# Optimization experiments

Hardware: AMD Instinct MI355X
Metric: run time of the kernel (lower is better)

Reference implementation:

```python
import jax, jax.numpy as jnp
import numpy as np

EPS = 1e-12      # F.normalize eps
BN_EPS = 1e-5    # BatchNorm1d eps


def _l2norm(x):
    # x: (B, E, S); normalize over channel dim E (torch F.normalize default dim=1)
    n = jnp.sqrt(jnp.sum(x * x, axis=1, keepdims=True))
    return x / jnp.maximum(n, EPS)


def _conv1x1(w, b, x):
    # 1x1 Conv1d: w (O, E), b (O,), x (B, S, E) -> (B, O, S)
    return jnp.einsum('oe,bse->bos', w, x) + b[None, :, None]


def _batchnorm(x, g, b):
    # train-mode BatchNorm1d on (B, F): biased batch stats over dim 0
    m = jnp.mean(x, axis=0)
    v = jnp.var(x, axis=0)
    return (x - m) * jax.lax.rsqrt(v + BN_EPS) * g + b


def _pairwise(X, Y, wx, bx, wy, by, g, be, mxw, mxb, myw, myb):
    # X: (B, Sx, e), Y: (B, Sy, e)
    Xn = _l2norm(_conv1x1(wx, bx, X))           # (B, E, Sx)
    Yn = _l2norm(_conv1x1(wy, by, Y))           # (B, E, Sy)
    S = jnp.einsum('bex,bey->bxy', Xn, Yn)       # (B, Sx, Sy)
    B, Sx, Sy = S.shape
    S = _batchnorm(S.reshape(B, Sx * Sy), g, be).reshape(B, Sx, Sy)
    potX = jnp.einsum('y,bxy->bx', mxw, S) + mxb  # margin_X: Conv1d(Sy,1,1)
    potY = jnp.einsum('x,bxy->by', myw, S) + myb  # margin_Y: Conv1d(Sx,1,1)
    return potX, potY


def _pairwise_self(X, wx, bx, wy, by, g, be, mxw, mxb):
    # Pairwise with Y=None: embed_X and embed_Y both applied to X; only X_poten returned
    Xn = _l2norm(_conv1x1(wx, bx, X))
    Yn = _l2norm(_conv1x1(wy, by, X))
    S = jnp.einsum('bex,bey->bxy', Xn, Yn)
    B, Sx, Sy = S.shape
    S = _batchnorm(S.reshape(B, Sx * Sy), g, be).reshape(B, Sx, Sy)
    return jnp.einsum('y,bxy->bx', mxw, S) + mxb


def _unary(X, w1, b1, w2, b2):
    # Unary: conv1d e->e, relu, (dropout=identity in eval), conv1d e->1
    h = jax.nn.relu(_conv1x1(w1, b1, X))         # (B, E, S)
    return jnp.einsum('e,bes->bs', w2, h) + b2


def _forward(utils, un_w1, un_b1, un_w2, un_b2,
             sp_wx, sp_bx, sp_wy, sp_by, sp_g, sp_b, sp_mxw, sp_mxb,
             pw_wx, pw_bx, pw_wy, pw_by, pw_g, pw_b, pw_mxw, pw_mxb, pw_myw, pw_myb,
             red_w):
    # utils: (3, B, S, e)
    unp = jax.vmap(_unary)(utils, un_w1, un_b1, un_w2, un_b2)                    # (3, B, S)
    sfp = jax.vmap(_pairwise_self)(utils, sp_wx, sp_bx, sp_wy, sp_by,
                                   sp_g, sp_b, sp_mxw, sp_mxb)                   # (3, B, S)
    # pairwise pairs in combinations order: (0,1), (0,2), (1,2)
    idx_i = jnp.array([0, 0, 1])
    idx_j = jnp.array([1, 2, 2])
    pX, pY = jax.vmap(_pairwise)(utils[idx_i], utils[idx_j],
                                 pw_wx, pw_bx, pw_wy, pw_by, pw_g, pw_b,
                                 pw_mxw, pw_mxb, pw_myw, pw_myb)                 # (3, B, S) each
    pots = [
        [unp[0], sfp[0], pX[0], pX[1]],   # util 0: ij of (0,1), ij of (0,2)
        [unp[1], sfp[1], pY[0], pX[2]],   # util 1: ji of (0,1), ij of (1,2)
        [unp[2], sfp[2], pY[1], pY[2]],   # util 2: ji of (0,2), ji of (1,2)
    ]
    outs = []
    for i in range(3):
        P = jnp.stack(pots[i], axis=1)                 # (B, 4, S)
        red = jnp.einsum('k,bks->bs', red_w[i], P)     # Conv1d(4,1,1,bias=False)
        attn = jax.nn.softmax(red, axis=1)             # softmax over spatial dim
        outs.append(jnp.einsum('bse,bs->be', utils[i], attn))  # bmm(utils^T, attn)
    return jnp.stack(outs, axis=0)                     # (3, B, e)


def setup_inputs() -> dict:
    key = jax.random.key(0)
    ks = iter(jax.random.split(key, 32))
    def rn(shape, scale=0.05):
        return jax.random.normal(next(ks), shape, dtype=jnp.float32) * scale
    e, S, B, NU, NP = 128, 1024, 32, 3, 3
    F = S * S
    return dict(
        utils=rn((NU, B, S, e), 1.0),
        un_w1=rn((NU, e, e)), un_b1=rn((NU, e)), un_w2=rn((NU, e)), un_b2=rn((NU,)),
        sp_wx=rn((NU, e, e)), sp_bx=rn((NU, e)), sp_wy=rn((NU, e, e)), sp_by=rn((NU, e)),
        sp_g=jnp.ones((NU, F), jnp.float32), sp_b=jnp.zeros((NU, F), jnp.float32),
        sp_mxw=rn((NU, S)), sp_mxb=rn((NU,)),
        pw_wx=rn((NP, e, e)), pw_bx=rn((NP, e)), pw_wy=rn((NP, e, e)), pw_by=rn((NP, e)),
        pw_g=jnp.ones((NP, F), jnp.float32), pw_b=jnp.zeros((NP, F), jnp.float32),
        pw_mxw=rn((NP, S)), pw_mxb=rn((NP,)), pw_myw=rn((NP, S)), pw_myb=rn((NP,)),
        red_w=rn((NU, 4)),
    )


def reference(utils, un_w1, un_b1, un_w2, un_b2,
              sp_wx, sp_bx, sp_wy, sp_by, sp_g, sp_b, sp_mxw, sp_mxb,
              pw_wx, pw_bx, pw_wy, pw_by, pw_g, pw_b, pw_mxw, pw_mxb, pw_myw, pw_myb,
              red_w):
    return _forward(utils, un_w1, un_b1, un_w2, un_b2,
                    sp_wx, sp_bx, sp_wy, sp_by, sp_g, sp_b, sp_mxw, sp_mxb,
                    pw_wx, pw_bx, pw_wy, pw_by, pw_g, pw_b, pw_mxw, pw_mxb, pw_myw, pw_myb,
                    red_w)
```

## Files before the change

kernel.cpp:

```cpp
#include <hip/hip_runtime.h>
#include <math.h>

constexpr int EE = 128;
constexpr int NS = 1024;
constexpr int NB = 32;
constexpr size_t BSE = (size_t)NB * NS * EE;

typedef __attribute__((ext_vector_type(4))) float f32x4;
typedef __attribute__((ext_vector_type(8))) short s16x8;
typedef __attribute__((ext_vector_type(4))) short s16x4;
typedef __attribute__((ext_vector_type(8))) __bf16 bf16v8;

__device__ __forceinline__ f32x4 mfma16(s16x8 a, s16x8 b, f32x4 c) {
  return __builtin_amdgcn_mfma_f32_16x16x32_bf16(
      __builtin_bit_cast(bf16v8, a), __builtin_bit_cast(bf16v8, b), c, 0, 0, 0);
}

__device__ __forceinline__ unsigned short f2bf(float f) {
  unsigned u = __builtin_bit_cast(unsigned, f);
  u += 0x7FFFu + ((u >> 16) & 1u);
  return (unsigned short)(u >> 16);
}
__device__ __forceinline__ float bf2f(unsigned short h) {
  unsigned u = ((unsigned)h) << 16;
  return __builtin_bit_cast(float, u);
}

__device__ __forceinline__ int swz(int b)  { return b ^ (((b >> 8) & 7) << 4); }
__device__ __forceinline__ int swz7(int b) { return b ^ (((b >> 7) & 7) << 4); }

__device__ __forceinline__ void gl_lds16(const void* gptr, void* lptr) {
  auto g = (const __attribute__((address_space(1))) unsigned int*)gptr;
  auto l = (__attribute__((address_space(3))) unsigned int*)lptr;
  __builtin_amdgcn_global_load_lds(g, l, 16, 0, 0);
}

__device__ __forceinline__ void stage32k(const char* gsrc, char* ldst, int wv, int lane) {
#pragma unroll
  for (int c = 0; c < 8; ++c) {
    int uoff = c*4096 + wv*1024;
    gl_lds16(gsrc + swz(uoff + lane*16), ldst + uoff);
  }
}

__device__ __forceinline__ void stage_half(const char* tile, char* ldst, int kh, int wv, int lane) {
#pragma unroll
  for (int c = 0; c < 4; ++c) {
    int uoff = c*4096 + wv*1024;
    int sa = swz7(uoff + lane*16);
    gl_lds16(tile + (sa >> 7)*256 + kh*128 + (sa & 127), ldst + uoff);
  }
}

constexpr size_t EMB_OFF   = 0;
constexpr size_t UNP_OFF   = EMB_OFF + 12ull * BSE * 2;
constexpr size_t SUMS_OFF  = UNP_OFF + 3ull * NB * NS * 4;
constexpr size_t SUMS2_OFF = SUMS_OFF + 6ull * NS * NS * 4;
constexpr size_t RB_OFF    = SUMS2_OFF + 6ull * NS * NS * 4;
constexpr size_t CX_OFF    = RB_OFF + 6ull * NS * NS * 2;
constexpr size_t POTX_OFF  = CX_OFF + 6ull * NS * 4;
constexpr size_t PYP_OFF   = POTX_OFF + 6ull * NB * NS * 4;
constexpr size_t CY_OFF    = PYP_OFF + 3ull * NB * 8 * NS * 4;

__global__ __launch_bounds__(256, 2) void embed_kernel(
    const float* __restrict__ utils,
    const float* __restrict__ un_w1, const float* __restrict__ un_b1,
    const float* __restrict__ un_w2, const float* __restrict__ un_b2,
    const float* __restrict__ sp_wx, const float* __restrict__ sp_bx,
    const float* __restrict__ sp_wy, const float* __restrict__ sp_by,
    const float* __restrict__ pw_wx, const float* __restrict__ pw_bx,
    const float* __restrict__ pw_wy, const float* __restrict__ pw_by,
    unsigned short* __restrict__ emb, float* __restrict__ unp)
{
  const int job = blockIdx.x >> 9;
  const int pt  = blockIdx.x & 511;
  const int u = job / 5, m = job % 5;

  const float* W; const float* bias;
  unsigned short* dst = nullptr;
  int mode;
  if (m == 0)      { W = un_w1 + u*EE*EE; bias = un_b1 + u*EE; mode = 0; }
  else if (m == 1) { W = sp_wx + u*EE*EE; bias = sp_bx + u*EE; dst = emb + (size_t)(2*u)*BSE;   mode = 1; }
  else if (m == 2) { W = sp_wy + u*EE*EE; bias = sp_by + u*EE; dst = emb + (size_t)(2*u+1)*BSE; mode = 1; }
  else {
    int q, side;
    if (u == 0)      { q = (m == 3) ? 0 : 1; side = 0; }
    else if (u == 1) { if (m == 3) { q = 0; side = 1; } else { q = 2; side = 0; } }
    else             { q = (m == 3) ? 1 : 2; side = 1; }
    W    = (side == 0 ? pw_wx : pw_wy) + q*EE*EE;
    bias = (side == 0 ? pw_bx : pw_by) + q*EE;
    dst  = emb + (size_t)(2*(3+q)+side)*BSE;
    mode = 1;
  }

  __shared__ short lA[64*128];
  __shared__ short lB[128*128];
  __shared__ float redbuf[64];

  const int t = threadIdx.x;
  {
    const char* src = (const char*)(utils + (size_t)u*BSE + (size_t)pt*64*EE);
#pragma unroll
    for (int c = 0; c < 8; ++c) {
      int off = c*4096 + t*16;
      float4 v = *(const float4*)(src + off);
      s16x4 h;
      h.x = (short)f2bf(v.x); h.y = (short)f2bf(v.y);
      h.z = (short)f2bf(v.z); h.w = (short)f2bf(v.w);
      *(s16x4*)((char*)lA + swz(off >> 1)) = h;
    }
    const char* wsrc = (const char*)W;
#pragma unroll
    for (int c = 0; c < 16; ++c) {
      int off = c*4096 + t*16;
      float4 v = *(const float4*)(wsrc + off);
      s16x4 h;
      h.x = (short)f2bf(v.x); h.y = (short)f2bf(v.y);
      h.z = (short)f2bf(v.z); h.w = (short)f2bf(v.w);
      *(s16x4*)((char*)lB + swz(off >> 1)) = h;
    }
  }
  __syncthreads();

  const int lane = t & 63, wv = t >> 6;
  const int wrE = wv & 1, wcE = wv >> 1;
  const int cL = lane & 15, r4 = (lane >> 4) * 4, k8 = (lane >> 4) * 8;

  f32x4 acc[2][4];
#pragma unroll
  for (int i = 0; i < 2; ++i)
#pragma unroll
    for (int j = 0; j < 4; ++j) acc[i][j] = f32x4{0.f, 0.f, 0.f, 0.f};

#pragma unroll
  for (int kk = 0; kk < 4; ++kk) {
    s16x8 av[2], bv[4];
#pragma unroll
    for (int i = 0; i < 2; ++i) {
      int row = wrE*32 + i*16 + cL;
      av[i] = *(const s16x8*)((const char*)lA + swz(row*256 + kk*64 + k8*2));
    }
#pragma unroll
    for (int j = 0; j < 4; ++j) {
      int row = wcE*64 + j*16 + cL;
      bv[j] = *(const s16x8*)((const char*)lB + swz(row*256 + kk*64 + k8*2));
    }
#pragma unroll
    for (int i = 0; i < 2; ++i)
#pragma unroll
      for (int j = 0; j < 4; ++j)
        acc[i][j] = mfma16(av[i], bv[j], acc[i][j]);
  }

  if (mode == 0) {
    const float* w2 = un_w2 + u*EE;
    float s[2][4];
#pragma unroll
    for (int i = 0; i < 2; ++i)
#pragma unroll
      for (int r = 0; r < 4; ++r) s[i][r] = 0.f;
#pragma unroll
    for (int i = 0; i < 2; ++i) {
#pragma unroll
      for (int j = 0; j < 4; ++j) {
        int o = wcE*64 + j*16 + cL;
        float bv2 = bias[o], w2v = w2[o];
#pragma unroll
        for (int r = 0; r < 4; ++r) {
          float v = acc[i][j][r] + bv2;
          v = v > 0.f ? v : 0.f;
          s[i][r] += v * w2v;
        }
      }
    }
#pragma unroll
    for (int msk = 1; msk < 16; msk <<= 1)
#pragma unroll
      for (int i = 0; i < 2; ++i)
#pragma unroll
        for (int r = 0; r < 4; ++r)
          s[i][r] += __shfl_xor(s[i][r], msk, 64);
    if (t < 64) redbuf[t] = 0.f;
    __syncthreads();
    if (cL == 0) {
#pragma unroll
      for (int i = 0; i < 2; ++i)
#pragma unroll
        for (int r = 0; r < 4; ++r)
          atomicAdd(&redbuf[wrE*32 + i*16 + r4 + r], s[i][r]);
    }
    __syncthreads();
    if (t < 64) unp[(size_t)u*NB*NS + (size_t)pt*64 + t] = redbuf[t] + un_b2[u];
  } else {
    float nrm[2][4];
#pragma unroll
    for (int i = 0; i < 2; ++i)
#pragma unroll
      for (int r = 0; r < 4; ++r) nrm[i][r] = 0.f;
#pragma unroll
    for (int i = 0; i < 2; ++i) {
#pragma unroll
      for (int j = 0; j < 4; ++j) {
        int o = wcE*64 + j*16 + cL;
        float bv2 = bias[o];
#pragma unroll
        for (int r = 0; r < 4; ++r) {
          acc[i][j][r] += bv2;
          nrm[i][r] += acc[i][j][r] * acc[i][j][r];
        }
      }
    }
#pragma unroll
    for (int msk = 1; msk < 16; msk <<= 1)
#pragma unroll
      for (int i = 0; i < 2; ++i)
#pragma unroll
        for (int r = 0; r < 4; ++r)
          nrm[i][r] += __shfl_xor(nrm[i][r], msk, 64);
    if (t < 64) redbuf[t] = 0.f;
    __syncthreads();
    if (cL == 0) {
#pragma unroll
      for (int i = 0; i < 2; ++i)
#pragma unroll
        for (int r = 0; r < 4; ++r)
          atomicAdd(&redbuf[wrE*32 + i*16 + r4 + r], nrm[i][r]);
    }
    __syncthreads();
#pragma unroll
    for (int i = 0; i < 2; ++i) {
#pragma unroll
      for (int r = 0; r < 4; ++r) {
        float n = redbuf[wrE*32 + i*16 + r4 + r];
        float sc = 1.f / fmaxf(sqrtf(n), 1e-12f);
        size_t pbase = ((size_t)pt*64 + wrE*32 + i*16 + r4 + r) * EE;
#pragma unroll
        for (int j = 0; j < 4; ++j) {
          int o = wcE*64 + j*16 + cL;
          dst[pbase + o] = f2bf(acc[i][j][r] * sc);
        }
      }
    }
  }
}

__global__ __launch_bounds__(256, 2) void pass1_kernel(
    const unsigned short* __restrict__ emb,
    float* __restrict__ sumS, float* __restrict__ sumS2)
{
  const int bid = blockIdx.x;
  const int p = bid >> 6, xt = (bid >> 3) & 7, yt = bid & 7;
  const char* Xe = (const char*)(emb + (size_t)(2*p)*BSE + (size_t)xt*128*EE);
  const char* Ye = (const char*)(emb + (size_t)(2*p+1)*BSE + (size_t)yt*128*EE);
  __shared__ char lds[65536];
  const int t = threadIdx.x, lane = t & 63, wv = t >> 6;
  const int wr = wv >> 1, wc = wv & 1, cL = lane & 15, r4 = (lane >> 4) * 4;
  const int q16 = (lane >> 4) * 16;

  f32x4 sS[4][4], sQ[4][4], acc[4][4];
#pragma unroll
  for (int i = 0; i < 4; ++i)
#pragma unroll
    for (int j = 0; j < 4; ++j) { sS[i][j] = f32x4{0.f,0.f,0.f,0.f}; sQ[i][j] = f32x4{0.f,0.f,0.f,0.f}; }

  stage_half(Xe, lds, 0, wv, lane);
  stage_half(Ye, lds + 16384, 0, wv, lane);
  __syncthreads();

  for (int s = 0; s < 2*NB; ++s) {
    const int cur = s & 1;
    const char* buf = lds + cur * 32768;
    if (s + 1 < 2*NB) {
      const int b1 = (s + 1) >> 1, kh1 = (s + 1) & 1;
      char* nb = lds + (cur ^ 1) * 32768;
      stage_half(Xe + (size_t)b1*NS*EE*2, nb, kh1, wv, lane);
      stage_half(Ye + (size_t)b1*NS*EE*2, nb + 16384, kh1, wv, lane);
    }
    if ((s & 1) == 0) {
#pragma unroll
      for (int i = 0; i < 4; ++i)
#pragma unroll
        for (int j = 0; j < 4; ++j) acc[i][j] = f32x4{0.f,0.f,0.f,0.f};
    }
#pragma unroll
    for (int kk2 = 0; kk2 < 2; ++kk2) {
      s16x8 av[4], bv[4];
#pragma unroll
      for (int i = 0; i < 4; ++i) {
        int row = wr*64 + i*16 + cL;
        av[i] = *(const s16x8*)(buf + swz7(row*128 + kk2*64 + q16));
      }
#pragma unroll
      for (int j = 0; j < 4; ++j) {
        int row = wc*64 + j*16 + cL;
        bv[j] = *(const s16x8*)(buf + 16384 + swz7(row*128 + kk2*64 + q16));
      }
#pragma unroll
      for (int i = 0; i < 4; ++i)
#pragma unroll
        for (int j = 0; j < 4; ++j)
          acc[i][j] = mfma16(av[i], bv[j], acc[i][j]);
    }
    if (s & 1) {
#pragma unroll
      for (int i = 0; i < 4; ++i)
#pragma unroll
        for (int j = 0; j < 4; ++j) {
          sS[i][j] += acc[i][j];
          sQ[i][j] += acc[i][j] * acc[i][j];
        }
    }
    __syncthreads();
  }
  float* oS = sumS  + (size_t)p * NS * NS;
  float* oQ = sumS2 + (size_t)p * NS * NS;
#pragma unroll
  for (int i = 0; i < 4; ++i)
#pragma unroll
    for (int j = 0; j < 4; ++j)
#pragma unroll
      for (int r = 0; r < 4; ++r) {
        int row = xt*128 + wr*64 + i*16 + r4 + r;
        int col = yt*128 + wc*64 + j*16 + cL;
        oS[(size_t)row*NS + col] = sS[i][j][r];
        oQ[(size_t)row*NS + col] = sQ[i][j][r];
      }
}

__global__ void stats_kernel(
    const float* __restrict__ sumS, const float* __restrict__ sumS2,
    const float* __restrict__ sp_g, const float* __restrict__ sp_b,
    const float* __restrict__ sp_mxw, const float* __restrict__ sp_mxb,
    const float* __restrict__ pw_g, const float* __restrict__ pw_b,
    const float* __restrict__ pw_mxw, const float* __restrict__ pw_mxb,
    unsigned short* __restrict__ Rb, float* __restrict__ cX)
{
  const int p = blockIdx.x >> 10, x = blockIdx.x & 1023, t = threadIdx.x;
  const float* g; const float* bb; const float* mxw; float mxb;
  if (p < 3) {
    g = sp_g + (size_t)p*NS*NS; bb = sp_b + (size_t)p*NS*NS;
    mxw = sp_mxw + p*NS; mxb = sp_mxb[p];
  } else {
    int q = p - 3;
    g = pw_g + (size_t)q*NS*NS; bb = pw_b + (size_t)q*NS*NS;
    mxw = pw_mxw + q*NS; mxb = pw_mxb[q];
  }
  const size_t ro = (size_t)p*NS*NS + (size_t)x*NS;
  const size_t gro = (size_t)x*NS;
  const int y = t * 4;
  float4 s4 = *(const float4*)(sumS + ro + y);
  float4 q4 = *(const float4*)(sumS2 + ro + y);
  float4 g4 = *(const float4*)(g + gro + y);
  float4 b4 = *(const float4*)(bb + gro + y);
  float4 m4 = *(const float4*)(mxw + y);
  float partial = 0.f;
  s16x4 rq;
  {
    const float inv = 1.f / 32.f;
    float sv[4] = {s4.x, s4.y, s4.z, s4.w};
    float qv[4] = {q4.x, q4.y, q4.z, q4.w};
    float gv[4] = {g4.x, g4.y, g4.z, g4.w};
    float bv[4] = {b4.x, b4.y, b4.z, b4.w};
    float mw[4] = {m4.x, m4.y, m4.z, m4.w};
#pragma unroll
    for (int c = 0; c < 4; ++c) {
      float mean = sv[c] * inv;
      float var  = qv[c] * inv - mean * mean;
      float rstd = rsqrtf(var + 1e-5f);
      unsigned short rh = f2bf(gv[c] * rstd);
      rq[c] = (short)rh;
      float Rq = bf2f(rh);
      partial += mw[c] * (bv[c] - Rq * mean);
    }
  }
  *(s16x4*)(Rb + ro + y) = rq;
  __shared__ float sred[256];
  sred[t] = partial;
  __syncthreads();
  if (t < 128) sred[t] += sred[t + 128];
  __syncthreads();
  if (t < 64) {
    float v = sred[t] + sred[t + 64];
#pragma unroll
    for (int msk = 1; msk < 64; msk <<= 1) v += __shfl_xor(v, msk, 64);
    if (t == 0) cX[p*NS + x] = v + mxb;
  }
}

__global__ __launch_bounds__(256, 4) void cy_kernel(
    const float* __restrict__ sumS, const unsigned short* __restrict__ Rb,
    const float* __restrict__ pw_b, const float* __restrict__ pw_myw,
    float* __restrict__ cY)
{
  const int q = blockIdx.x >> 4, ys = blockIdx.x & 15;
  const int p = q + 3;
  const int t = threadIdx.x, rg = t >> 6, c = t & 63;
  const int y = ys * 64 + c;
  const float* Sp = sumS + (size_t)p * NS * NS;
  const unsigned short* Rp = Rb + (size_t)p * NS * NS;
  const float* bbp = pw_b + (size_t)q * NS * NS;
  const float* myw = pw_myw + q * NS;
  const float inv = 1.f / 32.f;
  float acc = 0.f;
#pragma unroll 4
  for (int x = rg * 256; x < rg * 256 + 256; ++x) {
    float mw = myw[x];
    float mean = Sp[(size_t)x * NS + y] * inv;
    float R = bf2f(Rp[(size_t)x * NS + y]);
    float bbv = bbp[(size_t)x * NS + y];
    acc += mw * (bbv - R * mean);
  }
  __shared__ float red[256];
  red[t] = acc;
  __syncthreads();
  if (rg == 0)
    cY[(size_t)p * NS + y] = red[c] + red[64 + c] + red[128 + c] + red[192 + c];
}

__global__ __launch_bounds__(256, 2) void pass2_kernel(
    const unsigned short* __restrict__ emb, const unsigned short* __restrict__ Rb,
    const float* __restrict__ sp_mxw, const float* __restrict__ pw_mxw,
    const float* __restrict__ pw_myw,
    float* __restrict__ potX, float* __restrict__ potYpart)
{
  const int bid = blockIdx.x;
  const int p = bid >> 8, b = (bid >> 3) & 31, xt = bid & 7;
  const char* Ae = (const char*)(emb + (size_t)(2*p)*BSE + ((size_t)b*NS + (size_t)xt*128)*EE);
  const char* Be = (const char*)(emb + (size_t)(2*p+1)*BSE + (size_t)b*NS*EE);
  const unsigned short* Rp = Rb + (size_t)p*NS*NS;
  const float* mxw = (p < 3) ? (sp_mxw + p*NS) : (pw_mxw + (p-3)*NS);
  const float* myw = (p < 3) ? nullptr : (pw_myw + (p-3)*NS);
  __shared__ char lA[32768];
  __shared__ char lB[32768];
  __shared__ float pxbuf[128];
  __shared__ float pybuf[1024];
  const int t = threadIdx.x, lane = t & 63, wv = t >> 6;
  const int wr = wv >> 1, wc = wv & 1, cL = lane & 15, r4 = (lane >> 4) * 4, k8 = (lane >> 4) * 8;

  stage32k(Ae, lA, wv, lane);
  stage32k(Be, lB, wv, lane);
  if (t < 128) pxbuf[t] = 0.f;
#pragma unroll
  for (int k = 0; k < 4; ++k) pybuf[t + k*256] = 0.f;
  __syncthreads();

  float px[4][4];
#pragma unroll
  for (int i = 0; i < 4; ++i)
#pragma unroll
    for (int r = 0; r < 4; ++r) px[i][r] = 0.f;
  float mywv[4][4];
  if (myw) {
#pragma unroll
    for (int i = 0; i < 4; ++i)
#pragma unroll
      for (int r = 0; r < 4; ++r)
        mywv[i][r] = myw[xt*128 + wr*64 + i*16 + r4 + r];
  }

  for (int yt = 0; yt < 8; ++yt) {
    f32x4 acc[4][4];
#pragma unroll
    for (int i = 0; i < 4; ++i)
#pragma unroll
      for (int j = 0; j < 4; ++j) acc[i][j] = f32x4{0.f,0.f,0.f,0.f};
#pragma unroll
    for (int kk = 0; kk < 4; ++kk) {
      s16x8 av[4], bv[4];
#pragma unroll
      for (int i = 0; i < 4; ++i) {
        int row = wr*64 + i*16 + cL;
        av[i] = *(const s16x8*)(lA + swz(row*256 + kk*64 + k8*2));
      }
#pragma unroll
      for (int j = 0; j < 4; ++j) {
        int row = wc*64 + j*16 + cL;
        bv[j] = *(const s16x8*)(lB + swz(row*256 + kk*64 + k8*2));
      }
#pragma unroll
      for (int i = 0; i < 4; ++i)
#pragma unroll
        for (int j = 0; j < 4; ++j)
          acc[i][j] = mfma16(av[i], bv[j], acc[i][j]);
    }
    __syncthreads();

    float mxl[4];
#pragma unroll
    for (int j = 0; j < 4; ++j) mxl[j] = mxw[yt*128 + wc*64 + j*16 + cL];

    if (myw) {
      float py[4] = {0.f, 0.f, 0.f, 0.f};
#pragma unroll
      for (int i = 0; i < 4; ++i) {
#pragma unroll
        for (int r = 0; r < 4; ++r) {
          const unsigned short* Rr = Rp + (size_t)(xt*128 + wr*64 + i*16 + r4 + r)*NS + yt*128;
          float pxa = 0.f;
#pragma unroll
          for (int j = 0; j < 4; ++j) {
            float Rv = bf2f(Rr[wc*64 + j*16 + cL]);
            float tt = Rv * acc[i][j][r];
            pxa += mxl[j] * tt;
            py[j] += mywv[i][r] * tt;
          }
          px[i][r] += pxa;
        }
      }
#pragma unroll
      for (int j = 0; j < 4; ++j) {
        py[j] += __shfl_xor(py[j], 16, 64);
        py[j] += __shfl_xor(py[j], 32, 64);
      }
      if ((lane >> 4) == 0) {
#pragma unroll
        for (int j = 0; j < 4; ++j)
          atomicAdd(&pybuf[yt*128 + wc*64 + j*16 + cL], py[j]);
      }
    } else {
#pragma unroll
      for (int i = 0; i < 4; ++i) {
#pragma unroll
        for (int r = 0; r < 4; ++r) {
          const unsigned short* Rr = Rp + (size_t)(xt*128 + wr*64 + i*16 + r4 + r)*NS + yt*128;
          float pxa = 0.f;
#pragma unroll
          for (int j = 0; j < 4; ++j) {
            float Rv = bf2f(Rr[wc*64 + j*16 + cL]);
            pxa += mxl[j] * (Rv * acc[i][j][r]);
          }
          px[i][r] += pxa;
        }
      }
    }

    if (yt < 7)
      stage32k(Be + (size_t)(yt+1)*32768, lB, wv, lane);
    __syncthreads();
  }

#pragma unroll
  for (int msk = 1; msk < 16; msk <<= 1)
#pragma unroll
    for (int i = 0; i < 4; ++i)
#pragma unroll
      for (int r = 0; r < 4; ++r)
        px[i][r] += __shfl_xor(px[i][r], msk, 64);
  if (cL == 0) {
#pragma unroll
    for (int i = 0; i < 4; ++i)
#pragma unroll
      for (int r = 0; r < 4; ++r)
        atomicAdd(&pxbuf[wr*64 + i*16 + r4 + r], px[i][r]);
  }
  __syncthreads();
  if (t < 128) potX[((size_t)p*NB + b)*NS + (size_t)xt*128 + t] = pxbuf[t];

  if (myw) {
    const size_t base = ((size_t)((p-3)*NB + b) * 8 + xt) * NS;
#pragma unroll
    for (int k = 0; k < 4; ++k)
      potYpart[base + t + k*256] = pybuf[t + k*256];
  }
}

__global__ __launch_bounds__(256, 4) void final_kernel(
    const float* __restrict__ utils, const float* __restrict__ unp,
    const float* __restrict__ potX, const float* __restrict__ pyp,
    const float* __restrict__ cX, const float* __restrict__ cY,
    const float* __restrict__ pw_myb, const float* __restrict__ red_w,
    float* __restrict__ out)
{
  const int u = blockIdx.x >> 5, b = blockIdx.x & 31, t = threadIdx.x;
  const int lane = t & 63, wv = t >> 6;
  __shared__ float wts[1024];
  __shared__ float redA[4], redB[4];
  __shared__ float comb[128];
  const float* unpp  = unp  + ((size_t)u*NB + b)*NS;
  const float* selfX = potX + ((size_t)u*NB + b)*NS;
  const float* cXu   = cX + u*NS;
  const float rw0 = red_w[u*4+0], rw1 = red_w[u*4+1], rw2 = red_w[u*4+2], rw3 = red_w[u*4+3];

  int ty2, ty3; const float *x2 = nullptr, *x3 = nullptr, *c2, *c3;
  const float *y2 = nullptr, *y3 = nullptr; float a2 = 0.f, a3 = 0.f;
  if (u == 0) {
    ty2 = 0; x2 = potX + ((size_t)3*NB + b)*NS; c2 = cX + 3*NS;
    ty3 = 0; x3 = potX + ((size_t)4*NB + b)*NS; c3 = cX + 4*NS;
  } else if (u == 1) {
    ty2 = 1; y2 = pyp + ((size_t)(0*NB + b) * 8) * NS; c2 = cY + 3*NS; a2 = pw_myb[0];
    ty3 = 0; x3 = potX + ((size_t)5*NB + b)*NS; c3 = cX + 5*NS;
  } else {
    ty2 = 1; y2 = pyp + ((size_t)(1*NB + b) * 8) * NS; c2 = cY + 4*NS; a2 = pw_myb[1];
    ty3 = 1; y3 = pyp + ((size_t)(2*NB + b) * 8) * NS; c3 = cY + 5*NS; a3 = pw_myb[2];
  }
  float rv[4]; float lmax = -3.4e38f;
#pragma unroll
  for (int k = 0; k < 4; ++k) {
    int s = t*4 + k;
    float t2, t3;
    if (ty2 == 0) t2 = x2[s] + c2[s];
    else {
      float a = 0.f;
#pragma unroll
      for (int q = 0; q < 8; ++q) a += y2[(size_t)q*NS + s];
      t2 = a + c2[s] + a2;
    }
    if (ty3 == 0) t3 = x3[s] + c3[s];
    else {
      float a = 0.f;
#pragma unroll
      for (int q = 0; q < 8; ++q) a += y3[(size_t)q*NS + s];
      t3 = a + c3[s] + a3;
    }
    float v = rw0*unpp[s] + rw1*(selfX[s] + cXu[s]) + rw2*t2 + rw3*t3;
    rv[k] = v; lmax = fmaxf(lmax, v);
  }
#pragma unroll
  for (int msk = 1; msk < 64; msk <<= 1) lmax = fmaxf(lmax, __shfl_xor(lmax, msk, 64));
  if (lane == 0) redA[wv] = lmax;
  __syncthreads();
  const float gmax = fmaxf(fmaxf(redA[0], redA[1]), fmaxf(redA[2], redA[3]));
  float lsum = 0.f;
#pragma unroll
  for (int k = 0; k < 4; ++k) {
    float e2 = __expf(rv[k] - gmax);
    wts[t*4 + k] = e2; lsum += e2;
  }
#pragma unroll
  for (int msk = 1; msk < 64; msk <<= 1) lsum += __shfl_xor(lsum, msk, 64);
  if (lane == 0) redB[wv] = lsum;
  __syncthreads();
  const float inv = 1.f / (redB[0] + redB[1] + redB[2] + redB[3]);
  const int e = t & 127, half = t >> 7;
  const float* ub = utils + (size_t)u*BSE + (size_t)b*NS*EE;
  float acc = 0.f;
  const int s0 = half * 512;
#pragma unroll 8
  for (int s = s0; s < s0 + 512; ++s)
    acc += ub[(size_t)s*EE + e] * wts[s];
  if (half) comb[e] = acc;
  __syncthreads();
  if (!half) out[((size_t)u*NB + b)*EE + e] = (acc + comb[e]) * inv;
}

extern "C" void kernel_launch(void* const* d_in, const int* in_sizes, int n_in,
                              void* d_out, int out_size, void* d_ws, size_t ws_size,
                              hipStream_t stream)
{
  (void)in_sizes; (void)n_in; (void)out_size; (void)ws_size;
  const float* utils  = (const float*)d_in[0];
  const float* un_w1  = (const float*)d_in[1];
  const float* un_b1  = (const float*)d_in[2];
  const float* un_w2  = (const float*)d_in[3];
  const float* un_b2  = (const float*)d_in[4];
  const float* sp_wx  = (const float*)d_in[5];
  const float* sp_bx  = (const float*)d_in[6];
  const float* sp_wy  = (const float*)d_in[7];
  const float* sp_by  = (const float*)d_in[8];
  const float* sp_g   = (const float*)d_in[9];
  const float* sp_b   = (const float*)d_in[10];
  const float* sp_mxw = (const float*)d_in[11];
  const float* sp_mxb = (const float*)d_in[12];
  const float* pw_wx  = (const float*)d_in[13];
  const float* pw_bx  = (const float*)d_in[14];
  const float* pw_wy  = (const float*)d_in[15];
  const float* pw_by  = (const float*)d_in[16];
  const float* pw_g   = (const float*)d_in[17];
  const float* pw_b   = (const float*)d_in[18];
  const float* pw_mxw = (const float*)d_in[19];
  const float* pw_mxb = (const float*)d_in[20];
  const float* pw_myw = (const float*)d_in[21];
  const float* pw_myb = (const float*)d_in[22];
  const float* red_w  = (const float*)d_in[23];
  float* out = (float*)d_out;
  char* ws = (char*)d_ws;

  unsigned short* embp  = (unsigned short*)(ws + EMB_OFF);
  float* unpp           = (float*)(ws + UNP_OFF);
  float* sumSp          = (float*)(ws + SUMS_OFF);
  float* sumS2p         = (float*)(ws + SUMS2_OFF);
  unsigned short* Rbp   = (unsigned short*)(ws + RB_OFF);
  float* cXp            = (float*)(ws + CX_OFF);
  float* potXp          = (float*)(ws + POTX_OFF);
  float* pypp           = (float*)(ws + PYP_OFF);
  float* cYp            = (float*)(ws + CY_OFF);

  embed_kernel<<<dim3(7680), dim3(256), 0, stream>>>(
      utils, un_w1, un_b1, un_w2, un_b2, sp_wx, sp_bx, sp_wy, sp_by,
      pw_wx, pw_bx, pw_wy, pw_by, embp, unpp);
  pass1_kernel<<<dim3(384), dim3(256), 0, stream>>>(embp, sumSp, sumS2p);
  stats_kernel<<<dim3(6144), dim3(256), 0, stream>>>(
      sumSp, sumS2p, sp_g, sp_b, sp_mxw, sp_mxb,
      pw_g, pw_b, pw_mxw, pw_mxb, Rbp, cXp);
  cy_kernel<<<dim3(48), dim3(256), 0, stream>>>(
      sumSp, Rbp, pw_b, pw_myw, cYp);
  pass2_kernel<<<dim3(1536), dim3(256), 0, stream>>>(
      embp, Rbp, sp_mxw, pw_mxw, pw_myw, potXp, pypp);
  final_kernel<<<dim3(96), dim3(256), 0, stream>>>(
      utils, unpp, potXp, pypp, cXp, cYp, pw_myb, red_w, out);
}
```

Measured before the change: 317.5 us.

## Fuse BN stats into pass1 epilogue and loop embed jobs per block

The batch-norm statistics, the R matrix write and the cX/cY bias-term reductions are computed directly in the pass1 epilogue from register-held sums. This removes the full-size sumS/sumS2 buffers and the separate stats and cy kernels; a small cfin kernel adds up the per-tile partials. The embed kernel now loops over the five weight jobs per block, so the activation tile is loaded and converted once instead of five times. In exchange there are fewer embed blocks, so less parallelism, and more register pressure in the pass1 epilogue.

After: 270.8 us. 1.17x faster.

```diff
diff --git a/kernel.cpp b/kernel.cpp
--- a/kernel.cpp
+++ b/kernel.cpp
@@ -54,13 +54,13 @@
 
 constexpr size_t EMB_OFF   = 0;
 constexpr size_t UNP_OFF   = EMB_OFF + 12ull * BSE * 2;
-constexpr size_t SUMS_OFF  = UNP_OFF + 3ull * NB * NS * 4;
-constexpr size_t SUMS2_OFF = SUMS_OFF + 6ull * NS * NS * 4;
-constexpr size_t RB_OFF    = SUMS2_OFF + 6ull * NS * NS * 4;
+constexpr size_t RB_OFF    = UNP_OFF + 3ull * NB * NS * 4;
 constexpr size_t CX_OFF    = RB_OFF + 6ull * NS * NS * 2;
 constexpr size_t POTX_OFF  = CX_OFF + 6ull * NS * 4;
 constexpr size_t PYP_OFF   = POTX_OFF + 6ull * NB * NS * 4;
 constexpr size_t CY_OFF    = PYP_OFF + 3ull * NB * 8 * NS * 4;
+constexpr size_t CXP_OFF   = CY_OFF + 6ull * NS * 4;
+constexpr size_t CYP_OFF   = CXP_OFF + 6ull * 8 * NS * 4;
 
 __global__ __launch_bounds__(256, 2) void embed_kernel(
     const float* __restrict__ utils,
@@ -72,26 +72,8 @@
     const float* __restrict__ pw_wy, const float* __restrict__ pw_by,
     unsigned short* __restrict__ emb, float* __restrict__ unp)
 {
-  const int job = blockIdx.x >> 9;
-  const int pt  = blockIdx.x & 511;
-  const int u = job / 5, m = job % 5;
-
-  const float* W; const float* bias;
-  unsigned short* dst = nullptr;
-  int mode;
-  if (m == 0)      { W = un_w1 + u*EE*EE; bias = un_b1 + u*EE; mode = 0; }
-  else if (m == 1) { W = sp_wx + u*EE*EE; bias = sp_bx + u*EE; dst = emb + (size_t)(2*u)*BSE;   mode = 1; }
-  else if (m == 2) { W = sp_wy + u*EE*EE; bias = sp_by + u*EE; dst = emb + (size_t)(2*u+1)*BSE; mode = 1; }
-  else {
-    int q, side;
-    if (u == 0)      { q = (m == 3) ? 0 : 1; side = 0; }
-    else if (u == 1) { if (m == 3) { q = 0; side = 1; } else { q = 2; side = 0; } }
-    else             { q = (m == 3) ? 1 : 2; side = 1; }
-    W    = (side == 0 ? pw_wx : pw_wy) + q*EE*EE;
-    bias = (side == 0 ? pw_bx : pw_by) + q*EE;
-    dst  = emb + (size_t)(2*(3+q)+side)*BSE;
-    mode = 1;
-  }
+  const int u  = blockIdx.x >> 9;
+  const int pt = blockIdx.x & 511;
 
   __shared__ short lA[64*128];
   __shared__ short lB[128*128];
@@ -109,135 +91,158 @@
       h.z = (short)f2bf(v.z); h.w = (short)f2bf(v.w);
       *(s16x4*)((char*)lA + swz(off >> 1)) = h;
     }
-    const char* wsrc = (const char*)W;
-#pragma unroll
-    for (int c = 0; c < 16; ++c) {
-      int off = c*4096 + t*16;
-      float4 v = *(const float4*)(wsrc + off);
-      s16x4 h;
-      h.x = (short)f2bf(v.x); h.y = (short)f2bf(v.y);
-      h.z = (short)f2bf(v.z); h.w = (short)f2bf(v.w);
-      *(s16x4*)((char*)lB + swz(off >> 1)) = h;
-    }
-  }
-  __syncthreads();
+  }
 
   const int lane = t & 63, wv = t >> 6;
   const int wrE = wv & 1, wcE = wv >> 1;
   const int cL = lane & 15, r4 = (lane >> 4) * 4, k8 = (lane >> 4) * 8;
 
-  f32x4 acc[2][4];
-#pragma unroll
-  for (int i = 0; i < 2; ++i)
-#pragma unroll
-    for (int j = 0; j < 4; ++j) acc[i][j] = f32x4{0.f, 0.f, 0.f, 0.f};
-
-#pragma unroll
-  for (int kk = 0; kk < 4; ++kk) {
-    s16x8 av[2], bv[4];
-#pragma unroll
-    for (int i = 0; i < 2; ++i) {
-      int row = wrE*32 + i*16 + cL;
-      av[i] = *(const s16x8*)((const char*)lA + swz(row*256 + kk*64 + k8*2));
-    }
-#pragma unroll
-    for (int j = 0; j < 4; ++j) {
-      int row = wcE*64 + j*16 + cL;
-      bv[j] = *(const s16x8*)((const char*)lB + swz(row*256 + kk*64 + k8*2));
-    }
+  for (int m = 0; m < 5; ++m) {
+    const float* W; const float* bias;
+    unsigned short* dst = nullptr;
+    int mode;
+    if (m == 0)      { W = un_w1 + u*EE*EE; bias = un_b1 + u*EE; mode = 0; }
+    else if (m == 1) { W = sp_wx + u*EE*EE; bias = sp_bx + u*EE; dst = emb + (size_t)(2*u)*BSE;   mode = 1; }
+    else if (m == 2) { W = sp_wy + u*EE*EE; bias = sp_by + u*EE; dst = emb + (size_t)(2*u+1)*BSE; mode = 1; }
+    else {
+      int q, side;
+      if (u == 0)      { q = (m == 3) ? 0 : 1; side = 0; }
+      else if (u == 1) { if (m == 3) { q = 0; side = 1; } else { q = 2; side = 0; } }
+      else             { q = (m == 3) ? 1 : 2; side = 1; }
+      W    = (side == 0 ? pw_wx : pw_wy) + q*EE*EE;
+      bias = (side == 0 ? pw_bx : pw_by) + q*EE;
+      dst  = emb + (size_t)(2*(3+q)+side)*BSE;
+      mode = 1;
+    }
+
+    __syncthreads();
+    {
+      const char* wsrc = (const char*)W;
+#pragma unroll
+      for (int c = 0; c < 16; ++c) {
+        int off = c*4096 + t*16;
+        float4 v = *(const float4*)(wsrc + off);
+        s16x4 h;
+        h.x = (short)f2bf(v.x); h.y = (short)f2bf(v.y);
+        h.z = (short)f2bf(v.z); h.w = (short)f2bf(v.w);
+        *(s16x4*)((char*)lB + swz(off >> 1)) = h;
+      }
+    }
+    __syncthreads();
+
+    f32x4 acc[2][4];
 #pragma unroll
     for (int i = 0; i < 2; ++i)
 #pragma unroll
-      for (int j = 0; j < 4; ++j)
-        acc[i][j] = mfma16(av[i], bv[j], acc[i][j]);
-  }
-
-  if (mode == 0) {
-    const float* w2 = un_w2 + u*EE;
-    float s[2][4];
-#pragma unroll
-    for (int i = 0; i < 2; ++i)
-#pragma unroll
-      for (int r = 0; r < 4; ++r) s[i][r] = 0.f;
-#pragma unroll
-    for (int i = 0; i < 2; ++i) {
+      for (int j = 0; j < 4; ++j) acc[i][j] = f32x4{0.f, 0.f, 0.f, 0.f};
+
+#pragma unroll
+    for (int kk = 0; kk < 4; ++kk) {
+      s16x8 av[2], bv[4];
+#pragma unroll
+      for (int i = 0; i < 2; ++i) {
+        int row = wrE*32 + i*16 + cL;
+        av[i] = *(const s16x8*)((const char*)lA + swz(row*256 + kk*64 + k8*2));
+      }
 #pragma unroll
       for (int j = 0; j < 4; ++j) {
-        int o = wcE*64 + j*16 + cL;
-        float bv2 = bias[o], w2v = w2[o];
-#pragma unroll
-        for (int r = 0; r < 4; ++r) {
-          float v = acc[i][j][r] + bv2;
-          v = v > 0.f ? v : 0.f;
-          s[i][r] += v * w2v;
-        }
-      }
-    }
-#pragma unroll
-    for (int msk = 1; msk < 16; msk <<= 1)
+        int row = wcE*64 + j*16 + cL;
+        bv[j] = *(const s16x8*)((const char*)lB + swz(row*256 + kk*64 + k8*2));
+      }
 #pragma unroll
       for (int i = 0; i < 2; ++i)
 #pragma unroll
-        for (int r = 0; r < 4; ++r)
-          s[i][r] += __shfl_xor(s[i][r], msk, 64);
-    if (t < 64) redbuf[t] = 0.f;
-    __syncthreads();
-    if (cL == 0) {
+        for (int j = 0; j < 4; ++j)
+          acc[i][j] = mfma16(av[i], bv[j], acc[i][j]);
+    }
+
+    if (mode == 0) {
+      const float* w2 = un_w2 + u*EE;
+      float s[2][4];
 #pragma unroll
       for (int i = 0; i < 2; ++i)
 #pragma unroll
-        for (int r = 0; r < 4; ++r)
-          atomicAdd(&redbuf[wrE*32 + i*16 + r4 + r], s[i][r]);
-    }
-    __syncthreads();
-    if (t < 64) unp[(size_t)u*NB*NS + (size_t)pt*64 + t] = redbuf[t] + un_b2[u];
-  } else {
-    float nrm[2][4];
-#pragma unroll
-    for (int i = 0; i < 2; ++i)
-#pragma unroll
-      for (int r = 0; r < 4; ++r) nrm[i][r] = 0.f;
-#pragma unroll
-    for (int i = 0; i < 2; ++i) {
-#pragma unroll
-      for (int j = 0; j < 4; ++j) {
-        int o = wcE*64 + j*16 + cL;
-        float bv2 = bias[o];
-#pragma unroll
-        for (int r = 0; r < 4; ++r) {
-          acc[i][j][r] += bv2;
-          nrm[i][r] += acc[i][j][r] * acc[i][j][r];
-        }
-      }
-    }
-#pragma unroll
-    for (int msk = 1; msk < 16; msk <<= 1)
-#pragma unroll
-      for (int i = 0; i < 2; ++i)
-#pragma unroll
-        for (int r = 0; r < 4; ++r)
-          nrm[i][r] += __shfl_xor(nrm[i][r], msk, 64);
-    if (t < 64) redbuf[t] = 0.f;
-    __syncthreads();
-    if (cL == 0) {
-#pragma unroll
-      for (int i = 0; i < 2; ++i)
-#pragma unroll
-        for (int r = 0; r < 4; ++r)
-          atomicAdd(&redbuf[wrE*32 + i*16 + r4 + r], nrm[i][r]);
-    }
-    __syncthreads();
-#pragma unroll
-    for (int i = 0; i < 2; ++i) {
-#pragma unroll
-      for (int r = 0; r < 4; ++r) {
-        float n = redbuf[wrE*32 + i*16 + r4 + r];
-        float sc = 1.f / fmaxf(sqrtf(n), 1e-12f);
-        size_t pbase = ((size_t)pt*64 + wrE*32 + i*16 + r4 + r) * EE;
+        for (int r = 0; r < 4; ++r) s[i][r] = 0.f;
+#pragma unroll
+      for (int i = 0; i < 2; ++i) {
 #pragma unroll
         for (int j = 0; j < 4; ++j) {
           int o = wcE*64 + j*16 + cL;
-          dst[pbase + o] = f2bf(acc[i][j][r] * sc);
+          float bv2 = bias[o], w2v = w2[o];
+#pragma unroll
+          for (int r = 0; r < 4; ++r) {
+            float v = acc[i][j][r] + bv2;
+            v = v > 0.f ? v : 0.f;
+            s[i][r] += v * w2v;
+          }
+        }
+      }
+#pragma unroll
+      for (int msk = 1; msk < 16; msk <<= 1)
+#pragma unroll
+        for (int i = 0; i < 2; ++i)
+#pragma unroll
+          for (int r = 0; r < 4; ++r)
+            s[i][r] += __shfl_xor(s[i][r], msk, 64);
+      if (t < 64) redbuf[t] = 0.f;
+      __syncthreads();
+      if (cL == 0) {
+#pragma unroll
+        for (int i = 0; i < 2; ++i)
+#pragma unroll
+          for (int r = 0; r < 4; ++r)
+            atomicAdd(&redbuf[wrE*32 + i*16 + r4 + r], s[i][r]);
+      }
+      __syncthreads();
+      if (t < 64) unp[(size_t)u*NB*NS + (size_t)pt*64 + t] = redbuf[t] + un_b2[u];
+    } else {
+      float nrm[2][4];
+#pragma unroll
+      for (int i = 0; i < 2; ++i)
+#pragma unroll
+        for (int r = 0; r < 4; ++r) nrm[i][r] = 0.f;
+#pragma unroll
+      for (int i = 0; i < 2; ++i) {
+#pragma unroll
+        for (int j = 0; j < 4; ++j) {
+          int o = wcE*64 + j*16 + cL;
+          float bv2 = bias[o];
+#pragma unroll
+          for (int r = 0; r < 4; ++r) {
+            acc[i][j][r] += bv2;
+            nrm[i][r] += acc[i][j][r] * acc[i][j][r];
+          }
+        }
+      }
+#pragma unroll
+      for (int msk = 1; msk < 16; msk <<= 1)
+#pragma unroll
+        for (int i = 0; i < 2; ++i)
+#pragma unroll
+          for (int r = 0; r < 4; ++r)
+            nrm[i][r] += __shfl_xor(nrm[i][r], msk, 64);
+      if (t < 64) redbuf[t] = 0.f;
+      __syncthreads();
+      if (cL == 0) {
+#pragma unroll
+        for (int i = 0; i < 2; ++i)
+#pragma unroll
+          for (int r = 0; r < 4; ++r)
+            atomicAdd(&redbuf[wrE*32 + i*16 + r4 + r], nrm[i][r]);
+      }
+      __syncthreads();
+#pragma unroll
+      for (int i = 0; i < 2; ++i) {
+#pragma unroll
+        for (int r = 0; r < 4; ++r) {
+          float n = redbuf[wrE*32 + i*16 + r4 + r];
+          float sc = 1.f / fmaxf(sqrtf(n), 1e-12f);
+          size_t pbase = ((size_t)pt*64 + wrE*32 + i*16 + r4 + r) * EE;
+#pragma unroll
+          for (int j = 0; j < 4; ++j) {
+            int o = wcE*64 + j*16 + cL;
+            dst[pbase + o] = f2bf(acc[i][j][r] * sc);
+          }
         }
       }
     }
@@ -246,13 +251,20 @@
 
 __global__ __launch_bounds__(256, 2) void pass1_kernel(
     const unsigned short* __restrict__ emb,
-    float* __restrict__ sumS, float* __restrict__ sumS2)
+    const float* __restrict__ sp_g, const float* __restrict__ sp_b,
+    const float* __restrict__ sp_mxw,
+    const float* __restrict__ pw_g, const float* __restrict__ pw_b,
+    const float* __restrict__ pw_mxw, const float* __restrict__ pw_myw,
+    unsigned short* __restrict__ Rb, float* __restrict__ cXpart,
+    float* __restrict__ cYpart)
 {
   const int bid = blockIdx.x;
   const int p = bid >> 6, xt = (bid >> 3) & 7, yt = bid & 7;
   const char* Xe = (const char*)(emb + (size_t)(2*p)*BSE + (size_t)xt*128*EE);
   const char* Ye = (const char*)(emb + (size_t)(2*p+1)*BSE + (size_t)yt*128*EE);
   __shared__ char lds[65536];
+  __shared__ float cxbuf[128];
+  __shared__ float cybuf[128];
   const int t = threadIdx.x, lane = t & 63, wv = t >> 6;
   const int wr = wv >> 1, wc = wv & 1, cL = lane & 15, r4 = (lane >> 4) * 4;
   const int q16 = (lane >> 4) * 16;
@@ -265,6 +277,7 @@
 
   stage_half(Xe, lds, 0, wv, lane);
   stage_half(Ye, lds + 16384, 0, wv, lane);
+  if (t < 128) { cxbuf[t] = 0.f; cybuf[t] = 0.f; }
   __syncthreads();
 
   for (int s = 0; s < 2*NB; ++s) {
@@ -312,109 +325,87 @@
     }
     __syncthreads();
   }
-  float* oS = sumS  + (size_t)p * NS * NS;
-  float* oQ = sumS2 + (size_t)p * NS * NS;
-#pragma unroll
-  for (int i = 0; i < 4; ++i)
-#pragma unroll
-    for (int j = 0; j < 4; ++j)
-#pragma unroll
-      for (int r = 0; r < 4; ++r) {
-        int row = xt*128 + wr*64 + i*16 + r4 + r;
-        int col = yt*128 + wc*64 + j*16 + cL;
-        oS[(size_t)row*NS + col] = sS[i][j][r];
-        oQ[(size_t)row*NS + col] = sQ[i][j][r];
-      }
-}
-
-__global__ void stats_kernel(
-    const float* __restrict__ sumS, const float* __restrict__ sumS2,
-    const float* __restrict__ sp_g, const float* __restrict__ sp_b,
-    const float* __restrict__ sp_mxw, const float* __restrict__ sp_mxb,
-    const float* __restrict__ pw_g, const float* __restrict__ pw_b,
-    const float* __restrict__ pw_mxw, const float* __restrict__ pw_mxb,
-    unsigned short* __restrict__ Rb, float* __restrict__ cX)
+
+  const float* gp  = (p < 3) ? (sp_g + (size_t)p*NS*NS) : (pw_g + (size_t)(p-3)*NS*NS);
+  const float* bbp = (p < 3) ? (sp_b + (size_t)p*NS*NS) : (pw_b + (size_t)(p-3)*NS*NS);
+  const float* mxw = (p < 3) ? (sp_mxw + p*NS) : (pw_mxw + (p-3)*NS);
+  const float* myw = (p < 3) ? nullptr : (pw_myw + (p-3)*NS);
+  unsigned short* Rp = Rb + (size_t)p*NS*NS;
+  const float inv = 1.f / 32.f;
+
+  float mxl[4];
+#pragma unroll
+  for (int j = 0; j < 4; ++j) mxl[j] = mxw[yt*128 + wc*64 + j*16 + cL];
+  float mywr[4][4];
+  if (myw) {
+#pragma unroll
+    for (int i = 0; i < 4; ++i)
+#pragma unroll
+      for (int r = 0; r < 4; ++r)
+        mywr[i][r] = myw[xt*128 + wr*64 + i*16 + r4 + r];
+  }
+
+  float py[4] = {0.f, 0.f, 0.f, 0.f};
+#pragma unroll
+  for (int i = 0; i < 4; ++i) {
+#pragma unroll
+    for (int r = 0; r < 4; ++r) {
+      const size_t rowoff = (size_t)(xt*128 + wr*64 + i*16 + r4 + r)*NS + yt*128;
+      float cxv = 0.f;
+#pragma unroll
+      for (int j = 0; j < 4; ++j) {
+        int c = wc*64 + j*16 + cL;
+        float mean = sS[i][j][r] * inv;
+        float var  = sQ[i][j][r] * inv - mean * mean;
+        float rstd = rsqrtf(var + 1e-5f);
+        unsigned short rh = f2bf(gp[rowoff + c] * rstd);
+        Rp[rowoff + c] = rh;
+        float ct = bbp[rowoff + c] - bf2f(rh) * mean;
+        cxv += mxl[j] * ct;
+        if (myw) py[j] += mywr[i][r] * ct;
+      }
+      cxv += __shfl_xor(cxv, 1, 64);
+      cxv += __shfl_xor(cxv, 2, 64);
+      cxv += __shfl_xor(cxv, 4, 64);
+      cxv += __shfl_xor(cxv, 8, 64);
+      if (cL == 0) atomicAdd(&cxbuf[wr*64 + i*16 + r4 + r], cxv);
+    }
+  }
+  if (myw) {
+#pragma unroll
+    for (int j = 0; j < 4; ++j) {
+      py[j] += __shfl_xor(py[j], 16, 64);
+      py[j] += __shfl_xor(py[j], 32, 64);
+    }
+    if ((lane >> 4) == 0) {
+#pragma unroll
+      for (int j = 0; j < 4; ++j)
+        atomicAdd(&cybuf[wc*64 + j*16 + cL], py[j]);
+    }
+  }
+  __syncthreads();
+  if (t < 128) cXpart[((size_t)p*8 + yt)*NS + xt*128 + t] = cxbuf[t];
+  if (myw && t < 128) cYpart[((size_t)(p-3)*8 + xt)*NS + yt*128 + t] = cybuf[t];
+}
+
+__global__ void cfin_kernel(
+    const float* __restrict__ cXpart, const float* __restrict__ cYpart,
+    const float* __restrict__ sp_mxb, const float* __restrict__ pw_mxb,
+    float* __restrict__ cX, float* __restrict__ cY)
 {
-  const int p = blockIdx.x >> 10, x = blockIdx.x & 1023, t = threadIdx.x;
-  const float* g; const float* bb; const float* mxw; float mxb;
-  if (p < 3) {
-    g = sp_g + (size_t)p*NS*NS; bb = sp_b + (size_t)p*NS*NS;
-    mxw = sp_mxw + p*NS; mxb = sp_mxb[p];
-  } else {
-    int q = p - 3;
-    g = pw_g + (size_t)q*NS*NS; bb = pw_b + (size_t)q*NS*NS;
-    mxw = pw_mxw + q*NS; mxb = pw_mxb[q];
-  }
-  const size_t ro = (size_t)p*NS*NS + (size_t)x*NS;
-  const size_t gro = (size_t)x*NS;
-  const int y = t * 4;
-  float4 s4 = *(const float4*)(sumS + ro + y);
-  float4 q4 = *(const float4*)(sumS2 + ro + y);
-  float4 g4 = *(const float4*)(g + gro + y);
-  float4 b4 = *(const float4*)(bb + gro + y);
-  float4 m4 = *(const float4*)(mxw + y);
-  float partial = 0.f;
-  s16x4 rq;
-  {
-    const float inv = 1.f / 32.f;
-    float sv[4] = {s4.x, s4.y, s4.z, s4.w};
-    float qv[4] = {q4.x, q4.y, q4.z, q4.w};
-    float gv[4] = {g4.x, g4.y, g4.z, g4.w};
-    float bv[4] = {b4.x, b4.y, b4.z, b4.w};
-    float mw[4] = {m4.x, m4.y, m4.z, m4.w};
-#pragma unroll
-    for (int c = 0; c < 4; ++c) {
-      float mean = sv[c] * inv;
-      float var  = qv[c] * inv - mean * mean;
-      float rstd = rsqrtf(var + 1e-5f);
-      unsigned short rh = f2bf(gv[c] * rstd);
-      rq[c] = (short)rh;
-      float Rq = bf2f(rh);
-      partial += mw[c] * (bv[c] - Rq * mean);
-    }
-  }
-  *(s16x4*)(Rb + ro + y) = rq;
-  __shared__ float sred[256];
-  sred[t] = partial;
-  __syncthreads();
-  if (t < 128) sred[t] += sred[t + 128];
-  __syncthreads();
-  if (t < 64) {
-    float v = sred[t] + sred[t + 64];
-#pragma unroll
-    for (int msk = 1; msk < 64; msk <<= 1) v += __shfl_xor(v, msk, 64);
-    if (t == 0) cX[p*NS + x] = v + mxb;
-  }
-}
-
-__global__ __launch_bounds__(256, 4) void cy_kernel(
-    const float* __restrict__ sumS, const unsigned short* __restrict__ Rb,
-    const float* __restrict__ pw_b, const float* __restrict__ pw_myw,
-    float* __restrict__ cY)
-{
-  const int q = blockIdx.x >> 4, ys = blockIdx.x & 15;
-  const int p = q + 3;
-  const int t = threadIdx.x, rg = t >> 6, c = t & 63;
-  const int y = ys * 64 + c;
-  const float* Sp = sumS + (size_t)p * NS * NS;
-  const unsigned short* Rp = Rb + (size_t)p * NS * NS;
-  const float* bbp = pw_b + (size_t)q * NS * NS;
-  const float* myw = pw_myw + q * NS;
-  const float inv = 1.f / 32.f;
-  float acc = 0.f;
-#pragma unroll 4
-  for (int x = rg * 256; x < rg * 256 + 256; ++x) {
-    float mw = myw[x];
-    float mean = Sp[(size_t)x * NS + y] * inv;
-    float R = bf2f(Rp[(size_t)x * NS + y]);
-    float bbv = bbp[(size_t)x * NS + y];
-    acc += mw * (bbv - R * mean);
-  }
-  __shared__ float red[256];
-  red[t] = acc;
-  __syncthreads();
-  if (rg == 0)
-    cY[(size_t)p * NS + y] = red[c] + red[64 + c] + red[128 + c] + red[192 + c];
+  const int blk = blockIdx.x;
+  const int p = blk >> 2;
+  const int x = ((blk & 3) << 8) + threadIdx.x;
+  float a = 0.f;
+#pragma unroll
+  for (int yt = 0; yt < 8; ++yt) a += cXpart[((size_t)p*8 + yt)*NS + x];
+  cX[p*NS + x] = a + (p < 3 ? sp_mxb[p] : pw_mxb[p-3]);
+  if (p >= 3) {
+    float b = 0.f;
+#pragma unroll
+    for (int xt = 0; xt < 8; ++xt) b += cYpart[((size_t)(p-3)*8 + xt)*NS + x];
+    cY[p*NS + x] = b;
+  }
 }
 
 __global__ __launch_bounds__(256, 2) void pass2_kernel(
@@ -677,23 +668,22 @@
 
   unsigned short* embp  = (unsigned short*)(ws + EMB_OFF);
   float* unpp           = (float*)(ws + UNP_OFF);
-  float* sumSp          = (float*)(ws + SUMS_OFF);
-  float* sumS2p         = (float*)(ws + SUMS2_OFF);
   unsigned short* Rbp   = (unsigned short*)(ws + RB_OFF);
   float* cXp            = (float*)(ws + CX_OFF);
   float* potXp          = (float*)(ws + POTX_OFF);
   float* pypp           = (float*)(ws + PYP_OFF);
   float* cYp            = (float*)(ws + CY_OFF);
-
-  embed_kernel<<<dim3(7680), dim3(256), 0, stream>>>(
+  float* cXpartp        = (float*)(ws + CXP_OFF);
+  float* cYpartp        = (float*)(ws + CYP_OFF);
+
+  embed_kernel<<<dim3(1536), dim3(256), 0, stream>>>(
       utils, un_w1, un_b1, un_w2, un_b2, sp_wx, sp_bx, sp_wy, sp_by,
       pw_wx, pw_bx, pw_wy, pw_by, embp, unpp);
-  pass1_kernel<<<dim3(384), dim3(256), 0, stream>>>(embp, sumSp, sumS2p);
-  stats_kernel<<<dim3(6144), dim3(256), 0, stream>>>(
-      sumSp, sumS2p, sp_g, sp_b, sp_mxw, sp_mxb,
-      pw_g, pw_b, pw_mxw, pw_mxb, Rbp, cXp);
-  cy_kernel<<<dim3(48), dim3(256), 0, stream>>>(
-      sumSp, Rbp, pw_b, pw_myw, cYp);
+  pass1_kernel<<<dim3(384), dim3(256), 0, stream>>>(
+      embp, sp_g, sp_b, sp_mxw, pw_g, pw_b, pw_mxw, pw_myw,
+      Rbp, cXpartp, cYpartp);
+  cfin_kernel<<<dim3(24), dim3(256), 0, stream>>>(
+      cXpartp, cYpartp, sp_mxb, pw_mxb, cXp, cYp);
   pass2_kernel<<<dim3(1536), dim3(256), 0, stream>>>(
       embp, Rbp, sp_mxw, pw_mxw, pw_myw, potXp, pypp);
   final_kernel<<<dim3(96), dim3(256), 0, stream>>>(
```
